# Performance work log

Hardware: AMD Instinct MI355X
Metric: run time of the kernel (lower is better)

## Reference

```python
import jax, jax.numpy as jnp
import numpy as np

B, L, A = 512, 2048, 3  # batch, seq_len, num_atoms


def _batched_tmscore(pred, true, coord_mask, mask):
    """Batched masked Kabsch alignment + TM-score.

    pred, true: [B, L, A, 3] coordinates
    coord_mask: [B, L, A] bool (valid atoms)
    mask:       [B, L] bool (valid residues; sum gives n for d0 formula)
    returns:    [B] TM-score per sample
    """
    Bn = pred.shape[0]
    P = pred.reshape(Bn, -1, 3)   # [B, N, 3], N = L*A
    Q = true.reshape(Bn, -1, 3)
    w = coord_mask.reshape(Bn, -1).astype(pred.dtype)  # [B, N] binary weights
    cnt = jnp.sum(w, axis=-1)                          # [B] number of valid points
    cs = jnp.maximum(cnt, 1.0)[:, None, None]

    # masked centroids
    muP = jnp.sum(w[..., None] * P, axis=1, keepdims=True) / cs
    muQ = jnp.sum(w[..., None] * Q, axis=1, keepdims=True) / cs
    # center and zero-out invalid points (w is binary so w^2 == w)
    Pc = (P - muP) * w[..., None]
    Qc = (Q - muQ) * w[..., None]

    # cross-covariance [B, 3, 3] and batched SVD-based Kabsch rotation
    H = jnp.einsum('bni,bnj->bij', Pc, Qc)
    U, S, Vt = jnp.linalg.svd(H)
    det = jnp.sign(jnp.linalg.det(U) * jnp.linalg.det(Vt))  # reflection fix
    V = jnp.swapaxes(Vt, -1, -2)
    e = jnp.stack([jnp.ones_like(det), jnp.ones_like(det), det], axis=-1)  # [B,3]
    R = jnp.einsum('bik,bjk->bij', V * e[:, None, :], U)  # R = V diag(1,1,d) U^T

    # rotate pred onto true: aligned_j = R[j,i] * Pc_i
    aligned = jnp.einsum('bji,bni->bnj', R, Pc)
    dist2 = jnp.sum((aligned - Qc) ** 2, axis=-1)  # [B, N]; 0 at masked-out points

    # TM-score: d0 = 1.24*(n-15)^(1/3) - 1.8 with n = residue count
    n = jnp.sum(mask.astype(pred.dtype), axis=-1)  # [B]
    d0 = 1.24 * jnp.cbrt(jnp.maximum(n - 15.0, 1e-3)) - 1.8
    d0 = jnp.maximum(d0, 1e-3)
    tm_terms = 1.0 / (1.0 + dist2 / (d0 ** 2)[:, None])
    tm = jnp.sum(w * tm_terms, axis=-1) / jnp.maximum(cnt, 1.0)
    return jnp.where(cnt > 0, tm, 0.0)


def setup_inputs() -> dict:
    key = jax.random.key(0)
    k1, k2, k3, k4 = jax.random.split(key, 4)
    pred_points = jax.random.normal(k1, (B, L, A, 3), dtype=jnp.float32) * 10.0
    true_points = jax.random.normal(k2, (B, L, A, 3), dtype=jnp.float32) * 10.0
    mask = jax.random.bernoulli(k3, 0.9, (B, L))
    coord_mask = mask[..., None] & jax.random.bernoulli(k4, 0.95, (B, L, A))
    return {"pred_points": pred_points, "true_points": true_points,
            "coord_mask": coord_mask, "mask": mask}


def reference(pred_points, true_points, coord_mask, mask):
    return _batched_tmscore(pred_points, true_points, coord_mask, mask)
```

## Files before the change

### kernel.cpp

```cpp
#include <hip/hip_runtime.h>
#include <hip/hip_fp16.h>
#include <math.h>

#define BATCH 512
#define SEQL  2048
#define NPTS  (SEQL*3)
#define NFLT  (NPTS*3)
#define NGRP  (NPTS/4)
#define TPB   512
#define NWAVE (TPB/64)

__device__ __forceinline__ uint2 pack4(float4 v) {
    __half2 lo = __floats2half2_rn(v.x, v.y);
    __half2 hi = __floats2half2_rn(v.z, v.w);
    uint2 r;
    r.x = *(unsigned int*)&lo;
    r.y = *(unsigned int*)&hi;
    return r;
}
__device__ __forceinline__ float4 unpack4(uint2 u) {
    __half2 lo = *(__half2*)&u.x;
    __half2 hi = *(__half2*)&u.y;
    float2 a = __half22float2(lo);
    float2 b = __half22float2(hi);
    return make_float4(a.x, a.y, b.x, b.y);
}

__device__ __forceinline__ int detect_flag_wave(const void* cm) {
    unsigned int v = ((const unsigned int*)cm)[threadIdx.x & 63];
    bool wi = __all(v <= 1u);
    bool wb = __all((v & 0xFEFEFEFEu) == 0u);
    return wi ? 0 : (wb ? 1 : 2);
}

template <int K>
__device__ __forceinline__ void block_reduce(float* acc, float* lds) {
#pragma unroll
    for (int k = 0; k < K; ++k) {
#pragma unroll
        for (int off = 32; off > 0; off >>= 1)
            acc[k] += __shfl_down(acc[k], off, 64);
    }
    int lane = threadIdx.x & 63;
    int wid  = threadIdx.x >> 6;
    if (lane == 0) {
#pragma unroll
        for (int k = 0; k < K; ++k) lds[wid * K + k] = acc[k];
    }
    __syncthreads();
    if (threadIdx.x == 0) {
#pragma unroll
        for (int k = 0; k < K; ++k) {
            float s = 0.f;
#pragma unroll
            for (int w = 0; w < NWAVE; ++w) s += lds[w * K + k];
            acc[k] = s;
        }
    }
}

__device__ __forceinline__ void accum_pt(float* a, float w,
                                         float px, float py, float pz,
                                         float qx, float qy, float qz) {
    a[0] += w;
    float wpx = w * px, wpy = w * py, wpz = w * pz;
    a[1] += wpx; a[2] += wpy; a[3] += wpz;
    a[4] += w * qx; a[5] += w * qy; a[6] += w * qz;
    a[7]  += wpx * qx; a[8]  += wpx * qy; a[9]  += wpx * qz;
    a[10] += wpy * qx; a[11] += wpy * qy; a[12] += wpy * qz;
    a[13] += wpz * qx; a[14] += wpz * qy; a[15] += wpz * qz;
}

__device__ void kabsch_params(const float* s, float* o) {
    double cnt = (double)s[0];
    double cs = fmax(cnt, 1.0);
    double mup0 = (double)s[1] / cs, mup1 = (double)s[2] / cs, mup2 = (double)s[3] / cs;
    double muq0 = (double)s[4] / cs, muq1 = (double)s[5] / cs, muq2 = (double)s[6] / cs;

    double h00 = (double)s[7]  - cnt * mup0 * muq0;
    double h01 = (double)s[8]  - cnt * mup0 * muq1;
    double h02 = (double)s[9]  - cnt * mup0 * muq2;
    double h10 = (double)s[10] - cnt * mup1 * muq0;
    double h11 = (double)s[11] - cnt * mup1 * muq1;
    double h12 = (double)s[12] - cnt * mup1 * muq2;
    double h20 = (double)s[13] - cnt * mup2 * muq0;
    double h21 = (double)s[14] - cnt * mup2 * muq1;
    double h22 = (double)s[15] - cnt * mup2 * muq2;

    double a00 = h00*h00 + h10*h10 + h20*h20;
    double a01 = h00*h01 + h10*h11 + h20*h21;
    double a02 = h00*h02 + h10*h12 + h20*h22;
    double a11 = h01*h01 + h11*h11 + h21*h21;
    double a12 = h01*h02 + h11*h12 + h21*h22;
    double a22 = h02*h02 + h12*h12 + h22*h22;

    double q3  = (a00 + a11 + a22) / 3.0;
    double pp1 = a01*a01 + a02*a02 + a12*a12;
    double b00 = a00 - q3, b11 = a11 - q3, b22 = a22 - q3;
    double pp2 = b00*b00 + b11*b11 + b22*b22 + 2.0 * pp1;

    double l0, l1, l2;
    double v1x, v1y, v1z, v2x, v2y, v2z, v3x, v3y, v3z;
    if (pp2 <= 1e-24 * (q3 * q3) + 1e-290) {
        l0 = l1 = l2 = q3;
        v1x = 1; v1y = 0; v1z = 0;
        v2x = 0; v2y = 1; v2z = 0;
        v3x = 0; v3y = 0; v3z = 1;
    } else {
        double p = sqrt(pp2 / 6.0), invp = 1.0 / p;
        double c00 = b00*invp, c01 = a01*invp, c02 = a02*invp;
        double c11 = b11*invp, c12 = a12*invp, c22 = b22*invp;
        double detB = c00*(c11*c22 - c12*c12) - c01*(c01*c22 - c12*c02)
                    + c02*(c01*c12 - c11*c02);
        double r = fmin(1.0, fmax(-1.0, detB * 0.5));
        double phi = acos(r) / 3.0;
        l0 = q3 + 2.0 * p * cos(phi);
        l2 = q3 + 2.0 * p * cos(phi + 2.0943951023931953);
        l1 = 3.0 * q3 - l0 - l2;

        double aa00 = a00*a00 + a01*a01 + a02*a02;
        double aa01 = a00*a01 + a01*a11 + a02*a12;
        double aa02 = a00*a02 + a01*a12 + a02*a22;
        double aa11 = a01*a01 + a11*a11 + a12*a12;
        double aa12 = a01*a02 + a11*a12 + a12*a22;
        double aa22 = a02*a02 + a12*a12 + a22*a22;

        double s12 = l1 + l2, p12 = l1 * l2;
        double m00 = aa00 - s12*a00 + p12;
        double m01 = aa01 - s12*a01;
        double m02 = aa02 - s12*a02;
        double m11 = aa11 - s12*a11 + p12;
        double m12 = aa12 - s12*a12;
        double m22 = aa22 - s12*a22 + p12;
        double n0 = m00*m00 + m01*m01 + m02*m02;
        double n1 = m01*m01 + m11*m11 + m12*m12;
        double n2 = m02*m02 + m12*m12 + m22*m22;
        bool s0 = (n0 >= n1) && (n0 >= n2);
        bool sA = (n1 >= n2);
        v1x = s0 ? m00 : (sA ? m01 : m02);
        v1y = s0 ? m01 : (sA ? m11 : m12);
        v1z = s0 ? m02 : (sA ? m12 : m22);
        double n1v = sqrt(v1x*v1x + v1y*v1y + v1z*v1z);
        if (n1v > 1e-150) { v1x /= n1v; v1y /= n1v; v1z /= n1v; }
        else { v1x = 1; v1y = 0; v1z = 0; }

        double s01 = l0 + l1, p01 = l0 * l1;
        double t00 = aa00 - s01*a00 + p01;
        double t01 = aa01 - s01*a01;
        double t02 = aa02 - s01*a02;
        double t11 = aa11 - s01*a11 + p01;
        double t12 = aa12 - s01*a12;
        double t22 = aa22 - s01*a22 + p01;
        double u0n = t00*t00 + t01*t01 + t02*t02;
        double u1n = t01*t01 + t11*t11 + t12*t12;
        double u2n = t02*t02 + t12*t12 + t22*t22;
        bool d0c = (u0n >= u1n) && (u0n >= u2n);
        bool dA = (u1n >= u2n);
        v3x = d0c ? t00 : (dA ? t01 : t02);
        v3y = d0c ? t01 : (dA ? t11 : t12);
        v3z = d0c ? t02 : (dA ? t12 : t22);
        double dot13 = v3x*v1x + v3y*v1y + v3z*v1z;
        v3x -= dot13 * v1x; v3y -= dot13 * v1y; v3z -= dot13 * v1z;
        double n3v = sqrt(v3x*v3x + v3y*v3y + v3z*v3z);
        if (n3v > 1e-150) { v3x /= n3v; v3y /= n3v; v3z /= n3v; }
        else {
            double A0 = fabs(v1x), A1 = fabs(v1y), A2 = fabs(v1z);
            double axx = 0, axy = 0, axz = 0;
            if (A0 <= A1 && A0 <= A2) axx = 1; else if (A1 <= A2) axy = 1; else axz = 1;
            double dd = axx*v1x + axy*v1y + axz*v1z;
            v3x = axx - dd*v1x; v3y = axy - dd*v1y; v3z = axz - dd*v1z;
            double nn = sqrt(v3x*v3x + v3y*v3y + v3z*v3z);
            v3x /= nn; v3y /= nn; v3z /= nn;
        }
        v2x = v3y*v1z - v3z*v1y;
        v2y = v3z*v1x - v3x*v1z;
        v2z = v3x*v1y - v3y*v1x;
    }

    double sv0 = sqrt(fmax(l0, 0.0));
    double sv1 = sqrt(fmax(l1, 0.0));
    double sv2 = sqrt(fmax(l2, 0.0));
    double eps = sv0 * 1e-12 + 1e-300;

    double u0x, u0y, u0z, u1x, u1y, u1z, u2x, u2y, u2z;
    {
        double hx = h00*v1x + h01*v1y + h02*v1z;
        double hy = h10*v1x + h11*v1y + h12*v1z;
        double hz = h20*v1x + h21*v1y + h22*v1z;
        if (sv0 > eps) {
            double ix = hx / sv0, iy = hy / sv0, iz = hz / sv0;
            double nn = sqrt(ix*ix + iy*iy + iz*iz);
            if (nn > 1e-300) { ix /= nn; iy /= nn; iz /= nn; }
            u0x = ix; u0y = iy; u0z = iz;
        } else { u0x = 1; u0y = 0; u0z = 0; }
    }
    {
        double hx = h00*v2x + h01*v2y + h02*v2z;
        double hy = h10*v2x + h11*v2y + h12*v2z;
        double hz = h20*v2x + h21*v2y + h22*v2z;
        if (sv1 > eps) {
            double ix = hx / sv1, iy = hy / sv1, iz = hz / sv1;
            double nn = sqrt(ix*ix + iy*iy + iz*iz);
            if (nn > 1e-300) { ix /= nn; iy /= nn; iz /= nn; }
            u1x = ix; u1y = iy; u1z = iz;
        } else {
            double A0 = fabs(u0x), A1 = fabs(u0y), A2 = fabs(u0z);
            double axx = 0, axy = 0, axz = 0;
            if (A0 <= A1 && A0 <= A2) axx = 1; else if (A1 <= A2) axy = 1; else axz = 1;
            double cx = u0y*axz - u0z*axy;
            double cy = u0z*axx - u0x*axz;
            double cz = u0x*axy - u0y*axx;
            double nn = sqrt(cx*cx + cy*cy + cz*cz);
            if (nn > 1e-300) { cx /= nn; cy /= nn; cz /= nn; }
            u1x = cx; u1y = cy; u1z = cz;
        }
    }
    {
        double hx = h00*v3x + h01*v3y + h02*v3z;
        double hy = h10*v3x + h11*v3y + h12*v3z;
        double hz = h20*v3x + h21*v3y + h22*v3z;
        if (sv2 > eps) {
            double ix = hx / sv2, iy = hy / sv2, iz = hz / sv2;
            double nn = sqrt(ix*ix + iy*iy + iz*iz);
            if (nn > 1e-300) { ix /= nn; iy /= nn; iz /= nn; }
            u2x = ix; u2y = iy; u2z = iz;
        } else {
            u2x = u0y*u1z - u0z*u1y;
            u2y = u0z*u1x - u0x*u1z;
            u2z = u0x*u1y - u0y*u1x;
            double nn = sqrt(u2x*u2x + u2y*u2y + u2z*u2z);
            if (nn > 1e-300) { u2x /= nn; u2y /= nn; u2z /= nn; }
        }
    }

    double detH = h00*(h11*h22 - h12*h21) - h01*(h10*h22 - h12*h20)
                + h02*(h10*h21 - h11*h20);
    double e2 = (detH > 0.0) ? 1.0 : ((detH < 0.0) ? -1.0 : 0.0);

    double R00 = v1x*u0x + v2x*u1x + e2*v3x*u2x;
    double R01 = v1x*u0y + v2x*u1y + e2*v3x*u2y;
    double R02 = v1x*u0z + v2x*u1z + e2*v3x*u2z;
    double R10 = v1y*u0x + v2y*u1x + e2*v3y*u2x;
    double R11 = v1y*u0y + v2y*u1y + e2*v3y*u2y;
    double R12 = v1y*u0z + v2y*u1z + e2*v3y*u2z;
    double R20 = v1z*u0x + v2z*u1x + e2*v3z*u2x;
    double R21 = v1z*u0y + v2z*u1y + e2*v3z*u2y;
    double R22 = v1z*u0z + v2z*u1z + e2*v3z*u2z;

    o[0] = (float)R00; o[1] = (float)R01; o[2] = (float)R02;
    o[3] = (float)R10; o[4] = (float)R11; o[5] = (float)R12;
    o[6] = (float)R20; o[7] = (float)R21; o[8] = (float)R22;

    o[9]  = (float)(R00*mup0 + R01*mup1 + R02*mup2 - muq0);
    o[10] = (float)(R10*mup0 + R11*mup1 + R12*mup2 - muq1);
    o[11] = (float)(R20*mup0 + R21*mup1 + R22*mup2 - muq2);

    double n = (double)s[16];
    double d0 = 1.24 * cbrt(fmax(n - 15.0, 1e-3)) - 1.8;
    d0 = fmax(d0, 1e-3);
    o[12] = (float)(1.0 / (d0 * d0));
    o[13] = (float)cnt;
}

__global__ __launch_bounds__(TPB, 2) void k_fused(
    const float* __restrict__ P, const float* __restrict__ Q,
    const void* __restrict__ cmask, const void* __restrict__ rmask,
    float* __restrict__ out) {
    int b = blockIdx.x;
    int tid = threadIdx.x;
    __shared__ float lds[NWAVE * 17];
    __shared__ float prm[14];
    __shared__ uint2 sP0[NGRP], sP1[NGRP], sP2[NGRP];
    __shared__ uint2 sQ0[NGRP], sQ1[NGRP], sQ2[NGRP];
    int flag = detect_flag_wave(cmask);

    const float4* Pv = (const float4*)(P + (size_t)b * NFLT);
    const float4* Qv = (const float4*)(Q + (size_t)b * NFLT);
    size_t gbase = (size_t)b * NGRP;

    float4 p[9], q[9];
#pragma unroll
    for (int k = 0; k < 3; ++k) {
        int g = tid + k * TPB;
        p[3*k+0] = Pv[3*g+0]; p[3*k+1] = Pv[3*g+1]; p[3*k+2] = Pv[3*g+2];
        q[3*k+0] = Qv[3*g+0]; q[3*k+1] = Qv[3*g+1]; q[3*k+2] = Qv[3*g+2];
    }
    float w[12];
    float rescnt;
    {
        size_t rg = (size_t)b * (SEQL / 4) + tid;
        if (flag == 0) {
            const int4* cm4 = (const int4*)cmask;
            int4 m0 = cm4[gbase + tid], m1 = cm4[gbase + tid + TPB], m2 = cm4[gbase + tid + 2*TPB];
            int4 rv = ((const int4*)rmask)[rg];
            w[0]=m0.x?1.f:0.f; w[1]=m0.y?1.f:0.f; w[2]=m0.z?1.f:0.f; w[3]=m0.w?1.f:0.f;
            w[4]=m1.x?1.f:0.f; w[5]=m1.y?1.f:0.f; w[6]=m1.z?1.f:0.f; w[7]=m1.w?1.f:0.f;
            w[8]=m2.x?1.f:0.f; w[9]=m2.y?1.f:0.f; w[10]=m2.z?1.f:0.f; w[11]=m2.w?1.f:0.f;
            rescnt = (rv.x?1.f:0.f) + (rv.y?1.f:0.f) + (rv.z?1.f:0.f) + (rv.w?1.f:0.f);
        } else if (flag == 1) {
            const unsigned int* cmw = (const unsigned int*)cmask;
            unsigned int m0 = cmw[gbase + tid], m1 = cmw[gbase + tid + TPB], m2 = cmw[gbase + tid + 2*TPB];
            unsigned int rv = ((const unsigned int*)rmask)[rg];
            w[0]=(m0&0xFFu)?1.f:0.f; w[1]=(m0&0xFF00u)?1.f:0.f; w[2]=(m0&0xFF0000u)?1.f:0.f; w[3]=(m0&0xFF000000u)?1.f:0.f;
            w[4]=(m1&0xFFu)?1.f:0.f; w[5]=(m1&0xFF00u)?1.f:0.f; w[6]=(m1&0xFF0000u)?1.f:0.f; w[7]=(m1&0xFF000000u)?1.f:0.f;
            w[8]=(m2&0xFFu)?1.f:0.f; w[9]=(m2&0xFF00u)?1.f:0.f; w[10]=(m2&0xFF0000u)?1.f:0.f; w[11]=(m2&0xFF000000u)?1.f:0.f;
            rescnt = (float)__popc(rv);
        } else {
            const float4* cmf = (const float4*)cmask;
            float4 m0 = cmf[gbase + tid], m1 = cmf[gbase + tid + TPB], m2 = cmf[gbase + tid + 2*TPB];
            float4 rv = ((const float4*)rmask)[rg];
            w[0]=m0.x!=0.f?1.f:0.f; w[1]=m0.y!=0.f?1.f:0.f; w[2]=m0.z!=0.f?1.f:0.f; w[3]=m0.w!=0.f?1.f:0.f;
            w[4]=m1.x!=0.f?1.f:0.f; w[5]=m1.y!=0.f?1.f:0.f; w[6]=m1.z!=0.f?1.f:0.f; w[7]=m1.w!=0.f?1.f:0.f;
            w[8]=m2.x!=0.f?1.f:0.f; w[9]=m2.y!=0.f?1.f:0.f; w[10]=m2.z!=0.f?1.f:0.f; w[11]=m2.w!=0.f?1.f:0.f;
            rescnt = (rv.x!=0.f?1.f:0.f) + (rv.y!=0.f?1.f:0.f) + (rv.z!=0.f?1.f:0.f) + (rv.w!=0.f?1.f:0.f);
        }
    }

#pragma unroll
    for (int k = 0; k < 3; ++k) {
        int g = tid + k * TPB;
        sP0[g] = pack4(p[3*k+0]); sP1[g] = pack4(p[3*k+1]); sP2[g] = pack4(p[3*k+2]);
        sQ0[g] = pack4(q[3*k+0]); sQ1[g] = pack4(q[3*k+1]); sQ2[g] = pack4(q[3*k+2]);
    }

    float acc[17];
#pragma unroll
    for (int k = 0; k < 17; ++k) acc[k] = 0.0f;
    acc[16] = rescnt;

#pragma unroll
    for (int k = 0; k < 3; ++k) {
        float4 p0 = p[3*k+0], p1 = p[3*k+1], p2 = p[3*k+2];
        float4 q0 = q[3*k+0], q1 = q[3*k+1], q2 = q[3*k+2];
        accum_pt(acc, w[4*k+0], p0.x, p0.y, p0.z, q0.x, q0.y, q0.z);
        accum_pt(acc, w[4*k+1], p0.w, p1.x, p1.y, q0.w, q1.x, q1.y);
        accum_pt(acc, w[4*k+2], p1.z, p1.w, p2.x, q1.z, q1.w, q2.x);
        accum_pt(acc, w[4*k+3], p2.y, p2.z, p2.w, q2.y, q2.z, q2.w);
    }

    block_reduce<17>(acc, lds);

    if (tid == 0) kabsch_params(acc, prm);
    __syncthreads();

    float R0 = prm[0], R1 = prm[1], R2 = prm[2];
    float R3 = prm[3], R4 = prm[4], R5 = prm[5];
    float R6 = prm[6], R7 = prm[7], R8 = prm[8];
    float tx = prm[9], ty = prm[10], tz = prm[11];
    float inv = prm[12], cnt = prm[13];

    float acc2 = 0.0f;
#pragma unroll
    for (int k = 0; k < 3; ++k) {
        int g = tid + k * TPB;
        float4 p0 = unpack4(sP0[g]), p1 = unpack4(sP1[g]), p2 = unpack4(sP2[g]);
        float4 q0 = unpack4(sQ0[g]), q1 = unpack4(sQ1[g]), q2 = unpack4(sQ2[g]);
        float px[4] = {p0.x, p0.w, p1.z, p2.y};
        float py[4] = {p0.y, p1.x, p1.w, p2.z};
        float pz[4] = {p0.z, p1.y, p2.x, p2.w};
        float qx[4] = {q0.x, q0.w, q1.z, q2.y};
        float qy[4] = {q0.y, q1.x, q1.w, q2.z};
        float qz[4] = {q0.z, q1.y, q2.x, q2.w};
#pragma unroll
        for (int u = 0; u < 4; ++u) {
            float dx = R0*px[u] + R1*py[u] + R2*pz[u] - tx - qx[u];
            float dy = R3*px[u] + R4*py[u] + R5*pz[u] - ty - qy[u];
            float dz = R6*px[u] + R7*py[u] + R8*pz[u] - tz - qz[u];
            float d2 = dx*dx + dy*dy + dz*dz;
            acc2 += w[4*k+u] / (1.0f + d2 * inv);
        }
    }
    __syncthreads();
    float a2[1] = {acc2};
    block_reduce<1>(a2, lds);
    if (tid == 0)
        out[b] = (cnt > 0.0f) ? a2[0] / fmaxf(cnt, 1.0f) : 0.0f;
}

extern "C" void kernel_launch(void* const* d_in, const int* in_sizes, int n_in,
                              void* d_out, int out_size, void* d_ws, size_t ws_size,
                              hipStream_t stream) {
    const float* P = (const float*)d_in[0];
    const float* Q = (const float*)d_in[1];
    const void* cm = d_in[2];
    const void* rm = d_in[3];
    float* out = (float*)d_out;

    k_fused<<<BATCH, TPB, 0, stream>>>(P, Q, cm, rm, out);
}
```

Before: 29.21 us.

## Process two batch samples per block with a staged load/compute overlap

The kernel is restructured so each 512-thread block handles two batch samples and the grid is halved. The global loads for the second sample are issued after the first sample's reduction, overlapping the thread-0 Kabsch SVD work. Per-point mask weights are also packed into a 12-bit integer instead of a float array, to save registers. In exchange, the per-block LDS footprint doubles, which likely limits residency to one block per CU and serialises work that previously ran as two concurrent blocks.

```diff
diff --git a/kernel.cpp b/kernel.cpp
--- a/kernel.cpp
+++ b/kernel.cpp
@@ -262,119 +262,178 @@
     o[13] = (float)cnt;
 }
 
-__global__ __launch_bounds__(TPB, 2) void k_fused(
+__device__ __forceinline__ int load_batch(
     const float* __restrict__ P, const float* __restrict__ Q,
     const void* __restrict__ cmask, const void* __restrict__ rmask,
-    float* __restrict__ out) {
-    int b = blockIdx.x;
-    int tid = threadIdx.x;
-    __shared__ float lds[NWAVE * 17];
-    __shared__ float prm[14];
-    __shared__ uint2 sP0[NGRP], sP1[NGRP], sP2[NGRP];
-    __shared__ uint2 sQ0[NGRP], sQ1[NGRP], sQ2[NGRP];
-    int flag = detect_flag_wave(cmask);
-
+    int flag, int b, int tid, float4* p, float4* q, float* rescnt) {
     const float4* Pv = (const float4*)(P + (size_t)b * NFLT);
     const float4* Qv = (const float4*)(Q + (size_t)b * NFLT);
     size_t gbase = (size_t)b * NGRP;
-
-    float4 p[9], q[9];
+    size_t rg = (size_t)b * (SEQL / 4) + tid;
 #pragma unroll
     for (int k = 0; k < 3; ++k) {
         int g = tid + k * TPB;
         p[3*k+0] = Pv[3*g+0]; p[3*k+1] = Pv[3*g+1]; p[3*k+2] = Pv[3*g+2];
         q[3*k+0] = Qv[3*g+0]; q[3*k+1] = Qv[3*g+1]; q[3*k+2] = Qv[3*g+2];
     }
-    float w[12];
-    float rescnt;
-    {
-        size_t rg = (size_t)b * (SEQL / 4) + tid;
-        if (flag == 0) {
-            const int4* cm4 = (const int4*)cmask;
-            int4 m0 = cm4[gbase + tid], m1 = cm4[gbase + tid + TPB], m2 = cm4[gbase + tid + 2*TPB];
-            int4 rv = ((const int4*)rmask)[rg];
-            w[0]=m0.x?1.f:0.f; w[1]=m0.y?1.f:0.f; w[2]=m0.z?1.f:0.f; w[3]=m0.w?1.f:0.f;
-            w[4]=m1.x?1.f:0.f; w[5]=m1.y?1.f:0.f; w[6]=m1.z?1.f:0.f; w[7]=m1.w?1.f:0.f;
-            w[8]=m2.x?1.f:0.f; w[9]=m2.y?1.f:0.f; w[10]=m2.z?1.f:0.f; w[11]=m2.w?1.f:0.f;
-            rescnt = (rv.x?1.f:0.f) + (rv.y?1.f:0.f) + (rv.z?1.f:0.f) + (rv.w?1.f:0.f);
-        } else if (flag == 1) {
-            const unsigned int* cmw = (const unsigned int*)cmask;
-            unsigned int m0 = cmw[gbase + tid], m1 = cmw[gbase + tid + TPB], m2 = cmw[gbase + tid + 2*TPB];
-            unsigned int rv = ((const unsigned int*)rmask)[rg];
-            w[0]=(m0&0xFFu)?1.f:0.f; w[1]=(m0&0xFF00u)?1.f:0.f; w[2]=(m0&0xFF0000u)?1.f:0.f; w[3]=(m0&0xFF000000u)?1.f:0.f;
-            w[4]=(m1&0xFFu)?1.f:0.f; w[5]=(m1&0xFF00u)?1.f:0.f; w[6]=(m1&0xFF0000u)?1.f:0.f; w[7]=(m1&0xFF000000u)?1.f:0.f;
-            w[8]=(m2&0xFFu)?1.f:0.f; w[9]=(m2&0xFF00u)?1.f:0.f; w[10]=(m2&0xFF0000u)?1.f:0.f; w[11]=(m2&0xFF000000u)?1.f:0.f;
-            rescnt = (float)__popc(rv);
-        } else {
-            const float4* cmf = (const float4*)cmask;
-            float4 m0 = cmf[gbase + tid], m1 = cmf[gbase + tid + TPB], m2 = cmf[gbase + tid + 2*TPB];
-            float4 rv = ((const float4*)rmask)[rg];
-            w[0]=m0.x!=0.f?1.f:0.f; w[1]=m0.y!=0.f?1.f:0.f; w[2]=m0.z!=0.f?1.f:0.f; w[3]=m0.w!=0.f?1.f:0.f;
-            w[4]=m1.x!=0.f?1.f:0.f; w[5]=m1.y!=0.f?1.f:0.f; w[6]=m1.z!=0.f?1.f:0.f; w[7]=m1.w!=0.f?1.f:0.f;
-            w[8]=m2.x!=0.f?1.f:0.f; w[9]=m2.y!=0.f?1.f:0.f; w[10]=m2.z!=0.f?1.f:0.f; w[11]=m2.w!=0.f?1.f:0.f;
-            rescnt = (rv.x!=0.f?1.f:0.f) + (rv.y!=0.f?1.f:0.f) + (rv.z!=0.f?1.f:0.f) + (rv.w!=0.f?1.f:0.f);
-        }
-    }
-
-#pragma unroll
-    for (int k = 0; k < 3; ++k) {
-        int g = tid + k * TPB;
-        sP0[g] = pack4(p[3*k+0]); sP1[g] = pack4(p[3*k+1]); sP2[g] = pack4(p[3*k+2]);
-        sQ0[g] = pack4(q[3*k+0]); sQ1[g] = pack4(q[3*k+1]); sQ2[g] = pack4(q[3*k+2]);
-    }
-
-    float acc[17];
+    int wbits = 0;
+    if (flag == 0) {
+        const int4* cm4 = (const int4*)cmask;
+        int4 m0 = cm4[gbase + tid], m1 = cm4[gbase + tid + TPB], m2 = cm4[gbase + tid + 2*TPB];
+        int4 rv = ((const int4*)rmask)[rg];
+        wbits = (m0.x?1:0)|(m0.y?2:0)|(m0.z?4:0)|(m0.w?8:0)
+              | (m1.x?16:0)|(m1.y?32:0)|(m1.z?64:0)|(m1.w?128:0)
+              | (m2.x?256:0)|(m2.y?512:0)|(m2.z?1024:0)|(m2.w?2048:0);
+        *rescnt = (rv.x?1.f:0.f)+(rv.y?1.f:0.f)+(rv.z?1.f:0.f)+(rv.w?1.f:0.f);
+    } else if (flag == 1) {
+        const unsigned int* cmw = (const unsigned int*)cmask;
+        unsigned int m0 = cmw[gbase + tid], m1 = cmw[gbase + tid + TPB], m2 = cmw[gbase + tid + 2*TPB];
+        unsigned int rv = ((const unsigned int*)rmask)[rg];
+        wbits = ((m0&0xFFu)?1:0)|((m0&0xFF00u)?2:0)|((m0&0xFF0000u)?4:0)|((m0&0xFF000000u)?8:0)
+              | ((m1&0xFFu)?16:0)|((m1&0xFF00u)?32:0)|((m1&0xFF0000u)?64:0)|((m1&0xFF000000u)?128:0)
+              | ((m2&0xFFu)?256:0)|((m2&0xFF00u)?512:0)|((m2&0xFF0000u)?1024:0)|((m2&0xFF000000u)?2048:0);
+        *rescnt = (float)__popc(rv);
+    } else {
+        const float4* cmf = (const float4*)cmask;
+        float4 m0 = cmf[gbase + tid], m1 = cmf[gbase + tid + TPB], m2 = cmf[gbase + tid + 2*TPB];
+        float4 rv = ((const float4*)rmask)[rg];
+        wbits = (m0.x!=0.f?1:0)|(m0.y!=0.f?2:0)|(m0.z!=0.f?4:0)|(m0.w!=0.f?8:0)
+              | (m1.x!=0.f?16:0)|(m1.y!=0.f?32:0)|(m1.z!=0.f?64:0)|(m1.w!=0.f?128:0)
+              | (m2.x!=0.f?256:0)|(m2.y!=0.f?512:0)|(m2.z!=0.f?1024:0)|(m2.w!=0.f?2048:0);
+        *rescnt = (rv.x!=0.f?1.f:0.f)+(rv.y!=0.f?1.f:0.f)+(rv.z!=0.f?1.f:0.f)+(rv.w!=0.f?1.f:0.f);
+    }
+    return wbits;
+}
+
+__device__ __forceinline__ void sums_from_regs(const float4* p, const float4* q,
+                                               int wbits, float rescnt, float* acc) {
 #pragma unroll
     for (int k = 0; k < 17; ++k) acc[k] = 0.0f;
     acc[16] = rescnt;
-
 #pragma unroll
     for (int k = 0; k < 3; ++k) {
         float4 p0 = p[3*k+0], p1 = p[3*k+1], p2 = p[3*k+2];
         float4 q0 = q[3*k+0], q1 = q[3*k+1], q2 = q[3*k+2];
-        accum_pt(acc, w[4*k+0], p0.x, p0.y, p0.z, q0.x, q0.y, q0.z);
-        accum_pt(acc, w[4*k+1], p0.w, p1.x, p1.y, q0.w, q1.x, q1.y);
-        accum_pt(acc, w[4*k+2], p1.z, p1.w, p2.x, q1.z, q1.w, q2.x);
-        accum_pt(acc, w[4*k+3], p2.y, p2.z, p2.w, q2.y, q2.z, q2.w);
-    }
-
-    block_reduce<17>(acc, lds);
-
-    if (tid == 0) kabsch_params(acc, prm);
-    __syncthreads();
-
-    float R0 = prm[0], R1 = prm[1], R2 = prm[2];
-    float R3 = prm[3], R4 = prm[4], R5 = prm[5];
-    float R6 = prm[6], R7 = prm[7], R8 = prm[8];
-    float tx = prm[9], ty = prm[10], tz = prm[11];
-    float inv = prm[12], cnt = prm[13];
-
-    float acc2 = 0.0f;
+        float w0 = (wbits >> (4*k+0)) & 1 ? 1.f : 0.f;
+        float w1 = (wbits >> (4*k+1)) & 1 ? 1.f : 0.f;
+        float w2 = (wbits >> (4*k+2)) & 1 ? 1.f : 0.f;
+        float w3 = (wbits >> (4*k+3)) & 1 ? 1.f : 0.f;
+        accum_pt(acc, w0, p0.x, p0.y, p0.z, q0.x, q0.y, q0.z);
+        accum_pt(acc, w1, p0.w, p1.x, p1.y, q0.w, q1.x, q1.y);
+        accum_pt(acc, w2, p1.z, p1.w, p2.x, q1.z, q1.w, q2.x);
+        accum_pt(acc, w3, p2.y, p2.z, p2.w, q2.y, q2.z, q2.w);
+    }
+}
+
+__global__ __launch_bounds__(TPB, 2) void k_fused2(
+    const float* __restrict__ P, const float* __restrict__ Q,
+    const void* __restrict__ cmask, const void* __restrict__ rmask,
+    float* __restrict__ out) {
+    int blk = blockIdx.x;
+    int tid = threadIdx.x;
+    int b0 = 2 * blk, b1 = 2 * blk + 1;
+    __shared__ float lds[2][NWAVE * 17];
+    __shared__ float prm[2][14];
+    __shared__ uint2 sP0[2][NGRP], sP1[2][NGRP], sP2[2][NGRP];
+    __shared__ uint2 sQ0[2][NGRP], sQ1[2][NGRP], sQ2[2][NGRP];
+    int flag = detect_flag_wave(cmask);
+
+    float4 p[9], q[9];
+    float rescnt;
+
+    int wb0 = load_batch(P, Q, cmask, rmask, flag, b0, tid, p, q, &rescnt);
 #pragma unroll
     for (int k = 0; k < 3; ++k) {
         int g = tid + k * TPB;
-        float4 p0 = unpack4(sP0[g]), p1 = unpack4(sP1[g]), p2 = unpack4(sP2[g]);
-        float4 q0 = unpack4(sQ0[g]), q1 = unpack4(sQ1[g]), q2 = unpack4(sQ2[g]);
-        float px[4] = {p0.x, p0.w, p1.z, p2.y};
-        float py[4] = {p0.y, p1.x, p1.w, p2.z};
-        float pz[4] = {p0.z, p1.y, p2.x, p2.w};
-        float qx[4] = {q0.x, q0.w, q1.z, q2.y};
-        float qy[4] = {q0.y, q1.x, q1.w, q2.z};
-        float qz[4] = {q0.z, q1.y, q2.x, q2.w};
-#pragma unroll
-        for (int u = 0; u < 4; ++u) {
-            float dx = R0*px[u] + R1*py[u] + R2*pz[u] - tx - qx[u];
-            float dy = R3*px[u] + R4*py[u] + R5*pz[u] - ty - qy[u];
-            float dz = R6*px[u] + R7*py[u] + R8*pz[u] - tz - qz[u];
-            float d2 = dx*dx + dy*dy + dz*dz;
-            acc2 += w[4*k+u] / (1.0f + d2 * inv);
-        }
-    }
-    __syncthreads();
-    float a2[1] = {acc2};
-    block_reduce<1>(a2, lds);
-    if (tid == 0)
-        out[b] = (cnt > 0.0f) ? a2[0] / fmaxf(cnt, 1.0f) : 0.0f;
+        sP0[0][g] = pack4(p[3*k+0]); sP1[0][g] = pack4(p[3*k+1]); sP2[0][g] = pack4(p[3*k+2]);
+        sQ0[0][g] = pack4(q[3*k+0]); sQ1[0][g] = pack4(q[3*k+1]); sQ2[0][g] = pack4(q[3*k+2]);
+    }
+    float acc[17];
+    sums_from_regs(p, q, wb0, rescnt, acc);
+    block_reduce<17>(acc, lds[0]);
+
+    int wb1 = load_batch(P, Q, cmask, rmask, flag, b1, tid, p, q, &rescnt);
+    if (tid == 0) kabsch_params(acc, prm[0]);
+
+#pragma unroll
+    for (int k = 0; k < 3; ++k) {
+        int g = tid + k * TPB;
+        sP0[1][g] = pack4(p[3*k+0]); sP1[1][g] = pack4(p[3*k+1]); sP2[1][g] = pack4(p[3*k+2]);
+        sQ0[1][g] = pack4(q[3*k+0]); sQ1[1][g] = pack4(q[3*k+1]); sQ2[1][g] = pack4(q[3*k+2]);
+    }
+    float acc1[17];
+    sums_from_regs(p, q, wb1, rescnt, acc1);
+    block_reduce<17>(acc1, lds[1]);
+
+    if (tid == 0) kabsch_params(acc1, prm[1]);
+
+    {
+        float R0 = prm[0][0], R1 = prm[0][1], R2 = prm[0][2];
+        float R3 = prm[0][3], R4 = prm[0][4], R5 = prm[0][5];
+        float R6 = prm[0][6], R7 = prm[0][7], R8 = prm[0][8];
+        float tx = prm[0][9], ty = prm[0][10], tz = prm[0][11];
+        float inv = prm[0][12], cnt = prm[0][13];
+        float a2 = 0.0f;
+#pragma unroll
+        for (int k = 0; k < 3; ++k) {
+            int g = tid + k * TPB;
+            float4 p0 = unpack4(sP0[0][g]), p1 = unpack4(sP1[0][g]), p2 = unpack4(sP2[0][g]);
+            float4 q0 = unpack4(sQ0[0][g]), q1 = unpack4(sQ1[0][g]), q2 = unpack4(sQ2[0][g]);
+            float px[4] = {p0.x, p0.w, p1.z, p2.y};
+            float py[4] = {p0.y, p1.x, p1.w, p2.z};
+            float pz[4] = {p0.z, p1.y, p2.x, p2.w};
+            float qx[4] = {q0.x, q0.w, q1.z, q2.y};
+            float qy[4] = {q0.y, q1.x, q1.w, q2.z};
+            float qz[4] = {q0.z, q1.y, q2.x, q2.w};
+#pragma unroll
+            for (int u = 0; u < 4; ++u) {
+                float wv = (wb0 >> (4*k+u)) & 1 ? 1.f : 0.f;
+                float dx = R0*px[u] + R1*py[u] + R2*pz[u] - tx - qx[u];
+                float dy = R3*px[u] + R4*py[u] + R5*pz[u] - ty - qy[u];
+                float dz = R6*px[u] + R7*py[u] + R8*pz[u] - tz - qz[u];
+                float d2 = dx*dx + dy*dy + dz*dz;
+                a2 += wv / (1.0f + d2 * inv);
+            }
+        }
+        float ar[1] = {a2};
+        block_reduce<1>(ar, lds[0]);
+        if (tid == 0)
+            out[b0] = (cnt > 0.0f) ? ar[0] / fmaxf(cnt, 1.0f) : 0.0f;
+    }
+
+    {
+        float R0 = prm[1][0], R1 = prm[1][1], R2 = prm[1][2];
+        float R3 = prm[1][3], R4 = prm[1][4], R5 = prm[1][5];
+        float R6 = prm[1][6], R7 = prm[1][7], R8 = prm[1][8];
+        float tx = prm[1][9], ty = prm[1][10], tz = prm[1][11];
+        float inv = prm[1][12], cnt = prm[1][13];
+        float a2 = 0.0f;
+#pragma unroll
+        for (int k = 0; k < 3; ++k) {
+            int g = tid + k * TPB;
+            float4 p0 = unpack4(sP0[1][g]), p1 = unpack4(sP1[1][g]), p2 = unpack4(sP2[1][g]);
+            float4 q0 = unpack4(sQ0[1][g]), q1 = unpack4(sQ1[1][g]), q2 = unpack4(sQ2[1][g]);
+            float px[4] = {p0.x, p0.w, p1.z, p2.y};
+            float py[4] = {p0.y, p1.x, p1.w, p2.z};
+            float pz[4] = {p0.z, p1.y, p2.x, p2.w};
+            float qx[4] = {q0.x, q0.w, q1.z, q2.y};
+            float qy[4] = {q0.y, q1.x, q1.w, q2.z};
+            float qz[4] = {q0.z, q1.y, q2.x, q2.w};
+#pragma unroll
+            for (int u = 0; u < 4; ++u) {
+                float wv = (wb1 >> (4*k+u)) & 1 ? 1.f : 0.f;
+                float dx = R0*px[u] + R1*py[u] + R2*pz[u] - tx - qx[u];
+                float dy = R3*px[u] + R4*py[u] + R5*pz[u] - ty - qy[u];
+                float dz = R6*px[u] + R7*py[u] + R8*pz[u] - tz - qz[u];
+                float d2 = dx*dx + dy*dy + dz*dz;
+                a2 += wv / (1.0f + d2 * inv);
+            }
+        }
+        float ar[1] = {a2};
+        block_reduce<1>(ar, lds[1]);
+        if (tid == 0)
+            out[b1] = (cnt > 0.0f) ? ar[0] / fmaxf(cnt, 1.0f) : 0.0f;
+    }
 }
 
 extern "C" void kernel_launch(void* const* d_in, const int* in_sizes, int n_in,
@@ -386,5 +445,5 @@
     const void* rm = d_in[3];
     float* out = (float*)d_out;
 
-    k_fused<<<BATCH, TPB, 0, stream>>>(P, Q, cm, rm, out);
-}
+    k_fused2<<<BATCH / 2, TPB, 0, stream>>>(P, Q, cm, rm, out);
+}
```

New measurement: 30.98 us. 1.06x slower.

## Coalesce coordinate loads through LDS transpose and keep points in registers

Applied to the files above, without the earlier changes.

Global loads of P and Q switch from strided per-thread triples of float4 to fully coalesced float4 loads (tid + k*TPB), staged through a shared float4 buffer and read back in per-thread triples. The fp16 shared-memory copy used for the second pass goes away; the second pass reuses the fp32 register values, which removes the half pack/unpack and its precision loss. The cost is extra barriers, two LDS round trips, and a large 72KB shared buffer that may limit blocks per CU. Register pressure also rises because p and q stay live across the Kabsch step.

```diff
diff --git a/kernel.cpp b/kernel.cpp
--- a/kernel.cpp
+++ b/kernel.cpp
@@ -1,30 +1,14 @@
 #include <hip/hip_runtime.h>
-#include <hip/hip_fp16.h>
 #include <math.h>
 
 #define BATCH 512
 #define SEQL  2048
 #define NPTS  (SEQL*3)
 #define NFLT  (NPTS*3)
+#define NV    (NFLT/4)
 #define NGRP  (NPTS/4)
 #define TPB   512
 #define NWAVE (TPB/64)
-
-__device__ __forceinline__ uint2 pack4(float4 v) {
-    __half2 lo = __floats2half2_rn(v.x, v.y);
-    __half2 hi = __floats2half2_rn(v.z, v.w);
-    uint2 r;
-    r.x = *(unsigned int*)&lo;
-    r.y = *(unsigned int*)&hi;
-    return r;
-}
-__device__ __forceinline__ float4 unpack4(uint2 u) {
-    __half2 lo = *(__half2*)&u.x;
-    __half2 hi = *(__half2*)&u.y;
-    float2 a = __half22float2(lo);
-    float2 b = __half22float2(hi);
-    return make_float4(a.x, a.y, b.x, b.y);
-}
 
 __device__ __forceinline__ int detect_flag_wave(const void* cm) {
     unsigned int v = ((const unsigned int*)cm)[threadIdx.x & 63];
@@ -268,23 +252,15 @@
     float* __restrict__ out) {
     int b = blockIdx.x;
     int tid = threadIdx.x;
+    __shared__ float4 sT[NV];
     __shared__ float lds[NWAVE * 17];
     __shared__ float prm[14];
-    __shared__ uint2 sP0[NGRP], sP1[NGRP], sP2[NGRP];
-    __shared__ uint2 sQ0[NGRP], sQ1[NGRP], sQ2[NGRP];
     int flag = detect_flag_wave(cmask);
 
     const float4* Pv = (const float4*)(P + (size_t)b * NFLT);
     const float4* Qv = (const float4*)(Q + (size_t)b * NFLT);
     size_t gbase = (size_t)b * NGRP;
 
-    float4 p[9], q[9];
-#pragma unroll
-    for (int k = 0; k < 3; ++k) {
-        int g = tid + k * TPB;
-        p[3*k+0] = Pv[3*g+0]; p[3*k+1] = Pv[3*g+1]; p[3*k+2] = Pv[3*g+2];
-        q[3*k+0] = Qv[3*g+0]; q[3*k+1] = Qv[3*g+1]; q[3*k+2] = Qv[3*g+2];
-    }
     float w[12];
     float rescnt;
     {
@@ -316,11 +292,30 @@
         }
     }
 
+    float4 t[9];
+#pragma unroll
+    for (int k = 0; k < 9; ++k) t[k] = Pv[tid + k * TPB];
+#pragma unroll
+    for (int k = 0; k < 9; ++k) sT[tid + k * TPB] = t[k];
+    __syncthreads();
+    float4 p[9];
 #pragma unroll
     for (int k = 0; k < 3; ++k) {
-        int g = tid + k * TPB;
-        sP0[g] = pack4(p[3*k+0]); sP1[g] = pack4(p[3*k+1]); sP2[g] = pack4(p[3*k+2]);
-        sQ0[g] = pack4(q[3*k+0]); sQ1[g] = pack4(q[3*k+1]); sQ2[g] = pack4(q[3*k+2]);
+        int g3 = 3 * (tid + k * TPB);
+        p[3*k+0] = sT[g3 + 0]; p[3*k+1] = sT[g3 + 1]; p[3*k+2] = sT[g3 + 2];
+    }
+    __syncthreads();
+
+#pragma unroll
+    for (int k = 0; k < 9; ++k) t[k] = Qv[tid + k * TPB];
+#pragma unroll
+    for (int k = 0; k < 9; ++k) sT[tid + k * TPB] = t[k];
+    __syncthreads();
+    float4 q[9];
+#pragma unroll
+    for (int k = 0; k < 3; ++k) {
+        int g3 = 3 * (tid + k * TPB);
+        q[3*k+0] = sT[g3 + 0]; q[3*k+1] = sT[g3 + 1]; q[3*k+2] = sT[g3 + 2];
     }
 
     float acc[17];
@@ -352,9 +347,8 @@
     float acc2 = 0.0f;
 #pragma unroll
     for (int k = 0; k < 3; ++k) {
-        int g = tid + k * TPB;
-        float4 p0 = unpack4(sP0[g]), p1 = unpack4(sP1[g]), p2 = unpack4(sP2[g]);
-        float4 q0 = unpack4(sQ0[g]), q1 = unpack4(sQ1[g]), q2 = unpack4(sQ2[g]);
+        float4 p0 = p[3*k+0], p1 = p[3*k+1], p2 = p[3*k+2];
+        float4 q0 = q[3*k+0], q1 = q[3*k+1], q2 = q[3*k+2];
         float px[4] = {p0.x, p0.w, p1.z, p2.y};
         float py[4] = {p0.y, p1.x, p1.w, p2.z};
         float pz[4] = {p0.z, p1.y, p2.x, p2.w};
@@ -370,7 +364,6 @@
             acc2 += w[4*k+u] / (1.0f + d2 * inv);
         }
     }
-    __syncthreads();
     float a2[1] = {acc2};
     block_reduce<1>(a2, lds);
     if (tid == 0)
```

After: 35.91 us. 1.23x slower.
